# Kernel optimization log

Measured on AMD Instinct MI355X. Metric: run time of the kernel, lower is better.

## Reference

```python
import jax, jax.numpy as jnp
import numpy as np

B, S, D, H = 2, 2048, 1024, 16
DK = D // H


def setup_inputs() -> dict:
    key = jax.random.key(0)
    ks = jax.random.split(key, 12)
    init = lambda k, shp: (jax.random.normal(k, shp, dtype=jnp.float32) * 0.02)
    return {
        'query': jax.random.normal(ks[0], (B, S, D), dtype=jnp.float32),
        'key_in': jax.random.normal(ks[1], (B, S, D), dtype=jnp.float32),
        'value': jax.random.normal(ks[2], (B, S, D), dtype=jnp.float32),
        'w_q': init(ks[3], (D, D)), 'b_q': jnp.zeros((D,), jnp.float32),
        'w_k': init(ks[4], (D, D)), 'b_k': jnp.zeros((D,), jnp.float32),
        'w_v': init(ks[5], (D, D)), 'b_v': jnp.zeros((D,), jnp.float32),
        'w_o': init(ks[6], (D, D)), 'b_o': jnp.zeros((D,), jnp.float32),
        'fuzzy_centers': jax.random.normal(ks[7], (H, 3), dtype=jnp.float32),
        'fuzzy_widths': jnp.ones((H, 3), jnp.float32),
        'temperature': jnp.ones((1,), jnp.float32),
    }


def reference(query, key_in, value, w_q, b_q, w_k, b_k, w_v, b_v, w_o, b_o,
              fuzzy_centers, fuzzy_widths, temperature):
    b, s, d = query.shape
    h, dk = H, DK
    proj = lambda x, w, bias: x @ w.T + bias
    # [b,s,d] -> [b,h,s,dk]
    Q = proj(query, w_q, b_q).reshape(b, s, h, dk).transpose(0, 2, 1, 3)
    K = proj(key_in, w_k, b_k).reshape(b, s, h, dk).transpose(0, 2, 1, 3)
    V = proj(value, w_v, b_v).reshape(b, s, h, dk).transpose(0, 2, 1, 3)
    scores = jnp.einsum('bhsd,bhtd->bhst', Q, K) / np.sqrt(dk).astype(np.float32)
    # Faithful to torch: every (head,func) gaussian is applied to ALL heads' scores,
    # so each score gets sum of h*3 memberships, divided by 3.
    c = fuzzy_centers.reshape(-1)
    w = fuzzy_widths.reshape(-1)
    fz = jnp.zeros_like(scores)
    for i in range(h * 3):  # small fixed loop over membership functions
        fz = fz + jnp.exp(-(scores - c[i]) ** 2 / (2.0 * w[i] ** 2))
    fz = (fz / 3.0) / temperature[0]
    attn = jax.nn.softmax(fz, axis=-1)
    attended = jnp.einsum('bhst,bhtd->bhsd', attn, V)
    attended = attended.transpose(0, 2, 1, 3).reshape(b, s, d)
    return attended @ w_o.T + b_o
```

## Files before the change

### kernel.cpp

```cpp
#include <hip/hip_runtime.h>
#include <hip/hip_bf16.h>


#define S_LEN 2048
#define DMODEL 1024
#define NHEAD 16
#define DKH 64
#define NLUT 2048
#define LUT_MIN (-10.0f)
#define LUT_MAX (10.0f)

typedef __attribute__((ext_vector_type(8))) short bfx8;
typedef __attribute__((ext_vector_type(4))) float fx4;
typedef __attribute__((ext_vector_type(16))) float fx16;
typedef __attribute__((ext_vector_type(4))) unsigned ux4;

__device__ __forceinline__ short f2bf(float x) {
    unsigned u = __builtin_bit_cast(unsigned, x);
    u = (u + 0x7fffu + ((u >> 16) & 1u)) >> 16;
    return (short)u;
}

__device__ __forceinline__ unsigned cvt_pk_bf16(float lo, float hi) {
    unsigned r;
    asm("v_cvt_pk_bf16_f32 %0, %1, %2" : "=v"(r) : "v"(lo), "v"(hi));
    return r;
}

__device__ __forceinline__ void plane_swap(unsigned& a, unsigned& b) {
    asm volatile("v_permlane32_swap_b32 %0, %1" : "+v"(a), "+v"(b));
}

__device__ __forceinline__ void stage8_f32(const float* __restrict__ src, short* dst) {
    float4 a = *(const float4*)(src);
    float4 b = *(const float4*)(src + 4);
    bfx8 r;
    r[0] = f2bf(a.x); r[1] = f2bf(a.y); r[2] = f2bf(a.z); r[3] = f2bf(a.w);
    r[4] = f2bf(b.x); r[5] = f2bf(b.y); r[6] = f2bf(b.z); r[7] = f2bf(b.w);
    *(bfx8*)dst = r;
}

__device__ __forceinline__ void gload_lds16(const void* g, void* l) {
    __builtin_amdgcn_global_load_lds(
        (const __attribute__((address_space(1))) unsigned int*)g,
        (__attribute__((address_space(3))) unsigned int*)l, 16, 0, 0);
}

__device__ void lut_slice(const float* __restrict__ centers, const float* __restrict__ widths,
                          const float* __restrict__ temp, unsigned* __restrict__ lutp,
                          int slice) {
    __shared__ float cs[48], iw[48];
    __shared__ float gsh[257];
    int tid = threadIdx.x;
    if (tid < 48) {
        cs[tid] = centers[tid];
        float w = widths[tid];
        iw[tid] = -0.5f / (w * w);
    }
    __syncthreads();
    float invT = 1.0f / temp[0];
    const float step = (LUT_MAX - LUT_MIN) / (float)(NLUT - 1);
    float bound = 16.0f * invT;
    int base = slice * 256;
    #pragma unroll 1
    for (int idx = tid; idx < 257; idx += 256) {
        int i = base + idx; if (i > NLUT - 1) i = NLUT - 1;
        float s = LUT_MIN + step * (float)i;
        float a = 0.0f;
        #pragma unroll
        for (int j = 0; j < 48; j++) {
            float d = s - cs[j];
            a += expf(d * d * iw[j]);
        }
        float fz = a * (1.0f / 3.0f) * invT;
        gsh[idx] = expf(fz - bound);
    }
    __syncthreads();
    float g0 = gsh[tid];
    unsigned lo = (unsigned short)f2bf(g0);
    unsigned hi = (unsigned short)f2bf(gsh[tid + 1] - g0);
    lutp[base + tid] = lo | (hi << 16);
}

__global__ void build_lut_pk(const float* centers, const float* widths,
                             const float* temp, unsigned* lutp) {
    lut_slice(centers, widths, temp, lutp, blockIdx.x);
}

__global__ void cast_bf16(const float* __restrict__ src, short* __restrict__ dst, int n8) {
    int i = blockIdx.x * 256 + threadIdx.x;
    if (i < n8) stage8_f32(src + (size_t)i * 8, dst + (size_t)i * 8);
}

__global__ void prep_all(const float* q, const float* kin, const float* v,
        const float* wq, const float* wk, const float* wv, const float* wo,
        short* xq, short* xk, short* xv,
        short* bwq, short* bwk, short* bwv, short* bwo,
        const float* centers, const float* widths, const float* temp,
        unsigned* lutp) {
    int bid = blockIdx.x;
    if (bid >= 1024) {
        lut_slice(centers, widths, temp, lutp, bid - 1024);
        return;
    }
    for (int vb = bid; vb < 8192; vb += 1024) {
        const float* src; short* dst; int blk;
        if (vb < 6144) {
            int y = vb >> 11; blk = vb & 2047;
            src = (y == 0) ? q : (y == 1) ? kin : v;
            dst = (y == 0) ? xq : (y == 1) ? xk : xv;
        } else {
            int y = (vb - 6144) >> 9; blk = (vb - 6144) & 511;
            src = (y == 0) ? wq : (y == 1) ? wk : (y == 2) ? wv : wo;
            dst = (y == 0) ? bwq : (y == 1) ? bwk : (y == 2) ? bwv : bwo;
        }
        size_t i = (size_t)blk * 256 + threadIdx.x;
        stage8_f32(src + i * 8, (short*)dst + i * 8);
    }
}

struct GemmJob {
    const short* A; const short* W; const float* bias;
    short* obf; float* of32; int mode; float scale;
};

__global__ __launch_bounds__(256, 3) void gemm128(GemmJob j0, GemmJob j1, GemmJob j2) {
    __shared__ __align__(16) short As[2][128 * 32];
    __shared__ __align__(16) short Bs[2][128 * 32];
    GemmJob jb = (blockIdx.z == 0) ? j0 : (blockIdx.z == 1) ? j1 : j2;
    int tid = threadIdx.x, wave = tid >> 6, lane = tid & 63, quad = lane >> 4, l15 = lane & 15;
    int m0 = blockIdx.y * 128, n0 = blockIdx.x * 128;
    int wm = (wave >> 1) * 64, wn = (wave & 1) * 64;

    fx4 acc[4][4];
    #pragma unroll
    for (int i = 0; i < 4; i++)
        #pragma unroll
        for (int j = 0; j < 4; j++)
            #pragma unroll
            for (int r = 0; r < 4; r++) acc[i][j][r] = 0.0f;

    int fc = (quad ^ ((l15 >> 1) & 3)) * 8;

    int srow[2], sgc[2];
    #pragma unroll
    for (int r = 0; r < 2; r++) {
        int slot = r * 256 + wave * 64 + lane;
        srow[r] = slot >> 2;
        sgc[r] = (slot & 3) ^ ((srow[r] >> 1) & 3);
    }

    auto stage = [&](int k0, int buf) {
        #pragma unroll
        for (int r = 0; r < 2; r++) {
            gload_lds16(jb.A + (size_t)(m0 + srow[r]) * DMODEL + k0 + sgc[r] * 8,
                        &As[buf][(r * 256 + wave * 64) * 8]);
            gload_lds16(jb.W + (size_t)(n0 + srow[r]) * DMODEL + k0 + sgc[r] * 8,
                        &Bs[buf][(r * 256 + wave * 64) * 8]);
        }
    };

    stage(0, 0);
    __syncthreads();
    int buf = 0;
    for (int k0 = 0; k0 < DMODEL; k0 += 32) {
        if (k0 + 32 < DMODEL) stage(k0 + 32, buf ^ 1);
        bfx8 af[4], bfr[4];
        #pragma unroll
        for (int i = 0; i < 4; i++) af[i] = *(const bfx8*)(&As[buf][(wm + i * 16 + l15) * 32 + fc]);
        #pragma unroll
        for (int j = 0; j < 4; j++) bfr[j] = *(const bfx8*)(&Bs[buf][(wn + j * 16 + l15) * 32 + fc]);
        #pragma unroll
        for (int i = 0; i < 4; i++)
            #pragma unroll
            for (int j = 0; j < 4; j++)
                acc[i][j] = __builtin_amdgcn_mfma_f32_16x16x32_bf16(af[i], bfr[j], acc[i][j], 0, 0, 0);
        __syncthreads();
        buf ^= 1;
    }

    #pragma unroll
    for (int j = 0; j < 4; j++) {
        int n = n0 + wn + j * 16 + l15;
        float bv = jb.bias[n];
        #pragma unroll
        for (int i = 0; i < 4; i++) {
            #pragma unroll
            for (int r = 0; r < 4; r++) {
                int m = m0 + wm + i * 16 + quad * 4 + r;
                float v = (acc[i][j][r] + bv) * jb.scale;
                if (jb.mode == 0) {
                    int b = m >> 11, s = m & 2047, h = n >> 6, dk = n & 63;
                    jb.obf[(((size_t)(b * NHEAD + h)) * S_LEN + s) * DKH + dk] = f2bf(v);
                } else if (jb.mode == 1) {
                    int b = m >> 11, s = m & 2047, h = n >> 6, dk = n & 63;
                    jb.obf[(((size_t)(b * NHEAD + h)) * DKH + dk) * S_LEN + s] = f2bf(v);
                } else {
                    jb.of32[(size_t)m * DMODEL + n] = v;
                }
            }
        }
    }
}

__global__ __launch_bounds__(256, 4) void flash_fuzzy(const short* __restrict__ Qb,
        const short* __restrict__ Kb, const short* __restrict__ VTb,
        const unsigned* __restrict__ lutg, short* __restrict__ AO) {
    __shared__ __align__(16) short Ks[64 * 64];
    __shared__ __align__(16) short Vs[64 * 64];
    __shared__ unsigned lut[NLUT];
    __shared__ float dbuf[128];

    int tid = threadIdx.x, wave = tid >> 6, lane = tid & 63;
    int l31 = lane & 31, hi = lane >> 5;
    int wq = wave >> 1, st = wave & 1;
    int q0 = blockIdx.x * 64, bh = blockIdx.y;
    const short* Qp = Qb + (size_t)bh * S_LEN * DKH;
    const short* Kp = Kb + (size_t)bh * S_LEN * DKH;
    const short* Vp = VTb + (size_t)bh * DKH * S_LEN;

    #pragma unroll
    for (int i = tid; i < NLUT / 4; i += 256)
        ((uint4*)lut)[i] = ((const uint4*)lutg)[i];

    bfx8 aq[4];
    #pragma unroll
    for (int ks = 0; ks < 4; ks++)
        aq[ks] = *(const bfx8*)(Qp + (size_t)(q0 + wq * 32 + l31) * DKH + ks * 16 + hi * 8);

    bfx8 ones;
    #pragma unroll
    for (int i = 0; i < 8; i++) ones[i] = (short)0x3F80;

    fx16 oacc[2];
    fx16 dacc;
    #pragma unroll
    for (int r = 0; r < 16; r++) dacc[r] = 0.0f;
    #pragma unroll
    for (int dt = 0; dt < 2; dt++)
        #pragma unroll
        for (int r = 0; r < 16; r++) oacc[dt][r] = 0.0f;

    const float invh = (float)(NLUT - 1) / (LUT_MAX - LUT_MIN);
    const float xoff = -LUT_MIN * invh;

    int srow[2], sgc[2];
    #pragma unroll
    for (int r = 0; r < 2; r++) {
        int slot = (wave * 2 + r) * 64 + lane;
        srow[r] = slot >> 3;
        sgc[r] = (slot & 7) ^ ((srow[r] ^ (srow[r] >> 3)) & 7);
    }

    int krow = st * 32 + l31;
    int kphi = (krow ^ (krow >> 3)) & 7;

    for (int t0 = 0; t0 < S_LEN; t0 += 64) {
        __syncthreads();
        #pragma unroll
        for (int r = 0; r < 2; r++) {
            gload_lds16(Kp + (size_t)(t0 + srow[r]) * DKH + sgc[r] * 8,
                        &Ks[((wave * 2 + r) * 64) * 8]);
            gload_lds16(Vp + (size_t)srow[r] * S_LEN + t0 + sgc[r] * 8,
                        &Vs[((wave * 2 + r) * 64) * 8]);
        }
        __syncthreads();

        fx16 sac;
        #pragma unroll
        for (int r = 0; r < 16; r++) sac[r] = 0.0f;
        #pragma unroll
        for (int ks = 0; ks < 4; ks++) {
            bfx8 kf = *(const bfx8*)(&Ks[krow * 64 + (((ks * 2 + hi) ^ kphi) * 8)]);
            sac = __builtin_amdgcn_mfma_f32_32x32x16_bf16(kf, aq[ks], sac, 0, 0, 0);
        }

        unsigned w[8];
        #pragma unroll
        for (int t = 0; t < 8; t++) {
            float pv[2];
            #pragma unroll
            for (int u = 0; u < 2; u++) {
                float s = sac[t * 2 + u];
                float x = fmaf(s, invh, xoff);
                x = __builtin_amdgcn_fmed3f(x, 0.0f, (float)(NLUT - 1));
                int j = (int)x;
                float f = x - (float)j;
                unsigned pr = lut[j];
                float v0 = __builtin_bit_cast(float, pr << 16);
                float dl = __builtin_bit_cast(float, pr & 0xffff0000u);
                pv[u] = fmaf(f, dl, v0);
            }
            w[t] = cvt_pk_bf16(pv[0], pv[1]);
        }

        plane_swap(w[0], w[2]); plane_swap(w[1], w[3]);
        plane_swap(w[4], w[6]); plane_swap(w[5], w[7]);
        ux4 b0v = {w[0], w[1], w[2], w[3]};
        ux4 b1v = {w[4], w[5], w[6], w[7]};
        bfx8 pb0 = __builtin_bit_cast(bfx8, b0v);
        bfx8 pb1 = __builtin_bit_cast(bfx8, b1v);

        #pragma unroll
        for (int dt = 0; dt < 2; dt++) {
            int row = dt * 32 + l31;
            int vphi = (row ^ (row >> 3)) & 7;
            bfx8 v0f = *(const bfx8*)(&Vs[row * 64 + (((st * 4 + 0 + hi) ^ vphi) * 8)]);
            bfx8 v1f = *(const bfx8*)(&Vs[row * 64 + (((st * 4 + 2 + hi) ^ vphi) * 8)]);
            oacc[dt] = __builtin_amdgcn_mfma_f32_32x32x16_bf16(v0f, pb0, oacc[dt], 0, 0, 0);
            oacc[dt] = __builtin_amdgcn_mfma_f32_32x32x16_bf16(v1f, pb1, oacc[dt], 0, 0, 0);
        }
        dacc = __builtin_amdgcn_mfma_f32_32x32x16_bf16(ones, pb0, dacc, 0, 0, 0);
        dacc = __builtin_amdgcn_mfma_f32_32x32x16_bf16(ones, pb1, dacc, 0, 0, 0);
    }

    float den = dacc[0];

    __syncthreads();
    float* obuf = (wq == 0) ? (float*)Ks : (float*)Vs;
    if (st == 1) {
        #pragma unroll
        for (int dt = 0; dt < 2; dt++)
            #pragma unroll
            for (int r = 0; r < 16; r++)
                obuf[(dt * 16 + r) * 64 + lane] = oacc[dt][r];
        dbuf[wq * 64 + lane] = den;
    }
    __syncthreads();
    if (st == 0) {
        float dtot = den + dbuf[wq * 64 + lane];
        int b = bh >> 4, h = bh & 15;
        #pragma unroll
        for (int dt = 0; dt < 2; dt++) {
            #pragma unroll
            for (int r = 0; r < 16; r++) {
                float o = oacc[dt][r] + obuf[(dt * 16 + r) * 64 + lane];
                int dk = dt * 32 + (r & 3) + 8 * (r >> 2) + 4 * hi;
                int q = q0 + wq * 32 + l31;
                AO[((size_t)(b * S_LEN + q)) * DMODEL + h * DKH + dk] = f2bf(o / dtot);
            }
        }
    }
}

extern "C" void kernel_launch(void* const* d_in, const int* in_sizes, int n_in,
                              void* d_out, int out_size, void* d_ws, size_t ws_size,
                              hipStream_t stream) {
    const float* query   = (const float*)d_in[0];
    const float* key_in  = (const float*)d_in[1];
    const float* value   = (const float*)d_in[2];
    const float* w_q     = (const float*)d_in[3];
    const float* b_q     = (const float*)d_in[4];
    const float* w_k     = (const float*)d_in[5];
    const float* b_k     = (const float*)d_in[6];
    const float* w_v     = (const float*)d_in[7];
    const float* b_v     = (const float*)d_in[8];
    const float* w_o     = (const float*)d_in[9];
    const float* b_o     = (const float*)d_in[10];
    const float* centers = (const float*)d_in[11];
    const float* widths  = (const float*)d_in[12];
    const float* temp    = (const float*)d_in[13];

    char* p = (char*)d_ws;
    auto alloc = [&](size_t bytes) -> void* {
        void* r = (void*)p;
        p += (bytes + 255) & ~(size_t)255;
        return r;
    };
    const size_t nBHSD = (size_t)2 * NHEAD * S_LEN * DKH;
    const size_t nW    = (size_t)DMODEL * DMODEL;
    unsigned* lutp = (unsigned*)alloc(NLUT * 4);
    short* Qb  = (short*)alloc(nBHSD * 2);
    short* Kb  = (short*)alloc(nBHSD * 2);
    short* VTb = (short*)alloc(nBHSD * 2);

    char* save = p;
    short* xq  = (short*)alloc(nBHSD * 2);
    short* xk  = (short*)alloc(nBHSD * 2);
    short* xv  = (short*)alloc(nBHSD * 2);
    short* bwq = (short*)alloc(nW * 2);
    short* bwk = (short*)alloc(nW * 2);
    short* bwv = (short*)alloc(nW * 2);
    short* bwo = (short*)alloc(nW * 2);
    bool fused = ((size_t)(p - (char*)d_ws) <= ws_size);

    dim3 blk(256);
    dim3 gq(8, 32, 3), g1(8, 32, 1), fg(32, 32);
    GemmJob JO;

    if (fused) {
        short* AO = xq;
        prep_all<<<dim3(1032), blk, 0, stream>>>(query, key_in, value, w_q, w_k, w_v, w_o,
                xq, xk, xv, bwq, bwk, bwv, bwo, centers, widths, temp, lutp);
        GemmJob JQ = {xq, bwq, b_q, Qb,  nullptr, 0, 0.125f};
        GemmJob JK = {xk, bwk, b_k, Kb,  nullptr, 0, 1.0f};
        GemmJob JV = {xv, bwv, b_v, VTb, nullptr, 1, 1.0f};
        gemm128<<<gq, blk, 0, stream>>>(JQ, JK, JV);
        flash_fuzzy<<<fg, blk, 0, stream>>>(Qb, Kb, VTb, lutp, AO);
        JO = {AO, bwo, b_o, nullptr, (float*)d_out, 2, 1.0f};
        gemm128<<<g1, blk, 0, stream>>>(JO, JO, JO);
    } else {
        p = save;
        short* xf = (short*)alloc(nBHSD * 2);
        short* wb = (short*)alloc(nW * 2);
        short* AO = xf;
        const int n8x = (int)(nBHSD / 8), n8w = (int)(nW / 8);
        dim3 cg((n8x + 255) / 256), cw((n8w + 255) / 256);
        build_lut_pk<<<dim3(8), blk, 0, stream>>>(centers, widths, temp, lutp);
        cast_bf16<<<cg, blk, 0, stream>>>(query, xf, n8x);
        cast_bf16<<<cw, blk, 0, stream>>>(w_q, wb, n8w);
        JO = {xf, wb, b_q, Qb, nullptr, 0, 0.125f};
        gemm128<<<g1, blk, 0, stream>>>(JO, JO, JO);
        cast_bf16<<<cg, blk, 0, stream>>>(key_in, xf, n8x);
        cast_bf16<<<cw, blk, 0, stream>>>(w_k, wb, n8w);
        JO = {xf, wb, b_k, Kb, nullptr, 0, 1.0f};
        gemm128<<<g1, blk, 0, stream>>>(JO, JO, JO);
        cast_bf16<<<cg, blk, 0, stream>>>(value, xf, n8x);
        cast_bf16<<<cw, blk, 0, stream>>>(w_v, wb, n8w);
        JO = {xf, wb, b_v, VTb, nullptr, 1, 1.0f};
        gemm128<<<g1, blk, 0, stream>>>(JO, JO, JO);
        flash_fuzzy<<<fg, blk, 0, stream>>>(Qb, Kb, VTb, lutp, AO);
        cast_bf16<<<cw, blk, 0, stream>>>(w_o, wb, n8w);
        JO = {AO, wb, b_o, nullptr, (float*)d_out, 2, 1.0f};
        gemm128<<<g1, blk, 0, stream>>>(JO, JO, JO);
    }
}
```

Before: 259.9 us.

## Split-K the output projection GEMM with atomic accumulation onto bias-initialized output

The output projection GEMM previously launched only 256 blocks (8x32), which underfills the GPU. It is now split along K into two halves (grid z=2, 512 blocks), and each half atomically adds its partial sums into the output. The prep kernel is extended to pre-fill the output with the bias so the atomic adds need no extra bias term. This trades extra fp32 atomic traffic, an extra output-initialization write, and non-deterministic summation order for higher occupancy in the final GEMM.

Result: slower. 273.5 us (+5.2%).

```diff
diff --git a/kernel.cpp b/kernel.cpp
--- a/kernel.cpp
+++ b/kernel.cpp
@@ -97,13 +97,20 @@
         short* xq, short* xk, short* xv,
         short* bwq, short* bwk, short* bwv, short* bwo,
         const float* centers, const float* widths, const float* temp,
-        unsigned* lutp) {
+        unsigned* lutp, const float* bo, float* out) {
     int bid = blockIdx.x;
     if (bid >= 1024) {
         lut_slice(centers, widths, temp, lutp, bid - 1024);
         return;
     }
-    for (int vb = bid; vb < 8192; vb += 1024) {
+    for (int vb = bid; vb < 10240; vb += 1024) {
+        if (vb >= 8192) {
+            size_t e = (size_t)(vb - 8192) * 2048 + threadIdx.x * 8;
+            int n0 = (threadIdx.x * 8) & 1023;
+            *(float4*)(out + e)     = *(const float4*)(bo + n0);
+            *(float4*)(out + e + 4) = *(const float4*)(bo + n0 + 4);
+            continue;
+        }
         const float* src; short* dst; int blk;
         if (vb < 6144) {
             int y = vb >> 11; blk = vb & 2047;
@@ -121,7 +128,7 @@
 
 struct GemmJob {
     const short* A; const short* W; const float* bias;
-    short* obf; float* of32; int mode; float scale;
+    short* obf; float* of32; int mode; float scale; int kb; int ke;
 };
 
 __global__ __launch_bounds__(256, 3) void gemm128(GemmJob j0, GemmJob j1, GemmJob j2) {
@@ -160,11 +167,11 @@
         }
     };
 
-    stage(0, 0);
+    stage(jb.kb, 0);
     __syncthreads();
     int buf = 0;
-    for (int k0 = 0; k0 < DMODEL; k0 += 32) {
-        if (k0 + 32 < DMODEL) stage(k0 + 32, buf ^ 1);
+    for (int k0 = jb.kb; k0 < jb.ke; k0 += 32) {
+        if (k0 + 32 < jb.ke) stage(k0 + 32, buf ^ 1);
         bfx8 af[4], bfr[4];
         #pragma unroll
         for (int i = 0; i < 4; i++) af[i] = *(const bfx8*)(&As[buf][(wm + i * 16 + l15) * 32 + fc]);
@@ -182,7 +189,7 @@
     #pragma unroll
     for (int j = 0; j < 4; j++) {
         int n = n0 + wn + j * 16 + l15;
-        float bv = jb.bias[n];
+        float bv = (jb.mode == 3) ? 0.0f : jb.bias[n];
         #pragma unroll
         for (int i = 0; i < 4; i++) {
             #pragma unroll
@@ -195,8 +202,10 @@
                 } else if (jb.mode == 1) {
                     int b = m >> 11, s = m & 2047, h = n >> 6, dk = n & 63;
                     jb.obf[(((size_t)(b * NHEAD + h)) * DKH + dk) * S_LEN + s] = f2bf(v);
+                } else if (jb.mode == 2) {
+                    jb.of32[(size_t)m * DMODEL + n] = v;
                 } else {
-                    jb.of32[(size_t)m * DMODEL + n] = v;
+                    atomicAdd(&jb.of32[(size_t)m * DMODEL + n], v);
                 }
             }
         }
@@ -385,20 +394,22 @@
     bool fused = ((size_t)(p - (char*)d_ws) <= ws_size);
 
     dim3 blk(256);
-    dim3 gq(8, 32, 3), g1(8, 32, 1), fg(32, 32);
+    dim3 gq(8, 32, 3), go(8, 32, 2), g1(8, 32, 1), fg(32, 32);
     GemmJob JO;
 
     if (fused) {
         short* AO = xq;
         prep_all<<<dim3(1032), blk, 0, stream>>>(query, key_in, value, w_q, w_k, w_v, w_o,
-                xq, xk, xv, bwq, bwk, bwv, bwo, centers, widths, temp, lutp);
-        GemmJob JQ = {xq, bwq, b_q, Qb,  nullptr, 0, 0.125f};
-        GemmJob JK = {xk, bwk, b_k, Kb,  nullptr, 0, 1.0f};
-        GemmJob JV = {xv, bwv, b_v, VTb, nullptr, 1, 1.0f};
+                xq, xk, xv, bwq, bwk, bwv, bwo, centers, widths, temp, lutp,
+                b_o, (float*)d_out);
+        GemmJob JQ = {xq, bwq, b_q, Qb,  nullptr, 0, 0.125f, 0, 1024};
+        GemmJob JK = {xk, bwk, b_k, Kb,  nullptr, 0, 1.0f, 0, 1024};
+        GemmJob JV = {xv, bwv, b_v, VTb, nullptr, 1, 1.0f, 0, 1024};
         gemm128<<<gq, blk, 0, stream>>>(JQ, JK, JV);
         flash_fuzzy<<<fg, blk, 0, stream>>>(Qb, Kb, VTb, lutp, AO);
-        JO = {AO, bwo, b_o, nullptr, (float*)d_out, 2, 1.0f};
-        gemm128<<<g1, blk, 0, stream>>>(JO, JO, JO);
+        GemmJob JO1 = {AO, bwo, b_o, nullptr, (float*)d_out, 3, 1.0f, 0, 512};
+        GemmJob JO2 = {AO, bwo, b_o, nullptr, (float*)d_out, 3, 1.0f, 512, 1024};
+        gemm128<<<go, blk, 0, stream>>>(JO1, JO2, JO1);
     } else {
         p = save;
         short* xf = (short*)alloc(nBHSD * 2);
@@ -409,19 +420,19 @@
         build_lut_pk<<<dim3(8), blk, 0, stream>>>(centers, widths, temp, lutp);
         cast_bf16<<<cg, blk, 0, stream>>>(query, xf, n8x);
         cast_bf16<<<cw, blk, 0, stream>>>(w_q, wb, n8w);
-        JO = {xf, wb, b_q, Qb, nullptr, 0, 0.125f};
+        JO = {xf, wb, b_q, Qb, nullptr, 0, 0.125f, 0, 1024};
         gemm128<<<g1, blk, 0, stream>>>(JO, JO, JO);
         cast_bf16<<<cg, blk, 0, stream>>>(key_in, xf, n8x);
         cast_bf16<<<cw, blk, 0, stream>>>(w_k, wb, n8w);
-        JO = {xf, wb, b_k, Kb, nullptr, 0, 1.0f};
+        JO = {xf, wb, b_k, Kb, nullptr, 0, 1.0f, 0, 1024};
         gemm128<<<g1, blk, 0, stream>>>(JO, JO, JO);
         cast_bf16<<<cg, blk, 0, stream>>>(value, xf, n8x);
         cast_bf16<<<cw, blk, 0, stream>>>(w_v, wb, n8w);
-        JO = {xf, wb, b_v, VTb, nullptr, 1, 1.0f};
+        JO = {xf, wb, b_v, VTb, nullptr, 1, 1.0f, 0, 1024};
         gemm128<<<g1, blk, 0, stream>>>(JO, JO, JO);
         flash_fuzzy<<<fg, blk, 0, stream>>>(Qb, Kb, VTb, lutp, AO);
         cast_bf16<<<cw, blk, 0, stream>>>(w_o, wb, n8w);
-        JO = {AO, wb, b_o, nullptr, (float*)d_out, 2, 1.0f};
+        JO = {AO, wb, b_o, nullptr, (float*)d_out, 2, 1.0f, 0, 1024};
         gemm128<<<g1, blk, 0, stream>>>(JO, JO, JO);
     }
 }
```
